# Optimization experiments

Hardware: AMD Instinct MI355X
Metric: run time of the kernel (lower is better)

Reference implementation:

```python
import jax, jax.numpy as jnp
import numpy as np

B, S, D, H, DFF = 2, 2048, 768, 12, 3072
DK = D // H
EPS = 1e-6


def setup_inputs() -> dict:
    key = jax.random.key(0)
    ks = jax.random.split(key, 12)
    n = lambda k, shp: jax.random.normal(k, shp, jnp.float32) * 0.02
    return {
        "x": jax.random.normal(ks[0], (B, S, D), jnp.float32),
        "mask": jax.random.randint(ks[1], (1, 1, S, S), 0, 2).astype(jnp.int32),
        "wq": n(ks[2], (D, D)), "bq": jnp.zeros((D,), jnp.float32),
        "wk": n(ks[3], (D, D)), "bk": jnp.zeros((D,), jnp.float32),
        "wv": n(ks[4], (D, D)), "bv": jnp.zeros((D,), jnp.float32),
        "wo": n(ks[5], (D, D)), "bo": jnp.zeros((D,), jnp.float32),
        "w1": n(ks[6], (D, DFF)), "b1": jnp.zeros((DFF,), jnp.float32),
        "w2": n(ks[7], (DFF, D)), "b2": jnp.zeros((D,), jnp.float32),
        "alpha1": jnp.ones((D,), jnp.float32), "beta1": jnp.zeros((D,), jnp.float32),
        "alpha2": jnp.ones((D,), jnp.float32), "beta2": jnp.zeros((D,), jnp.float32),
    }


def _layernorm(x, alpha, bias):
    # Faithful to source: unbiased std (ddof=1) and eps added to std, not var.
    mean = x.mean(axis=-1, keepdims=True)
    var = jnp.sum((x - mean) ** 2, axis=-1, keepdims=True) / (x.shape[-1] - 1)
    return alpha * (x - mean) / (jnp.sqrt(var) + EPS) + bias


def reference(x, mask, wq, bq, wk, bk, wv, bv, wo, bo, w1, b1, w2, b2,
              alpha1, beta1, alpha2, beta2):
    # --- residual 1: pre-norm self-attention ---
    h = _layernorm(x, alpha1, beta1)
    q = (h @ wq + bq).reshape(B, S, H, DK).transpose(0, 2, 1, 3)  # [B,H,S,DK]
    k = (h @ wk + bk).reshape(B, S, H, DK).transpose(0, 2, 1, 3)
    v = (h @ wv + bv).reshape(B, S, H, DK).transpose(0, 2, 1, 3)
    scores = jnp.einsum('bhsd,bhtd->bhst', q, k) / jnp.sqrt(jnp.float32(DK))
    scores = jnp.where(mask == 0, jnp.float32(-1e9), scores)
    attn = jax.nn.softmax(scores, axis=-1)
    o = jnp.einsum('bhst,bhtd->bhsd', attn, v)
    o = o.transpose(0, 2, 1, 3).reshape(B, S, D)
    x = x + (o @ wo + bo)
    # --- residual 2: pre-norm FFN ---
    h2 = _layernorm(x, alpha2, beta2)
    ff = jnp.maximum(h2 @ w1 + b1, 0.0) @ w2 + b2
    return x + ff
```

## Files before the change

### kernel.cpp

```cpp
#include <hip/hip_runtime.h>

typedef unsigned short u16;
typedef unsigned int u32;
typedef unsigned long long u64;
typedef __attribute__((ext_vector_type(8))) short bf16x8;
typedef __attribute__((ext_vector_type(4))) float f32x4;
typedef __attribute__((ext_vector_type(2))) unsigned int u32x2;

#define SEQ 2048
#define DM  768
#define NH  12
#define NB  2
#define LDQ (3 * DM)

#define SCALE_Q 0.180336879f
#define NEGB   -1.44269504e9f

__device__ __forceinline__ float bf2f(u16 u) {
  union { u32 i; float f; } v; v.i = ((u32)u) << 16; return v.f;
}
__device__ __forceinline__ u16 f2bf(float f) {
  union { float f; u32 i; } v; v.f = f;
  u32 r = v.i + 0x7FFFu + ((v.i >> 16) & 1u);
  return (u16)(r >> 16);
}
__device__ __forceinline__ void gl_lds16(const u16* g, u16* l) {
  __builtin_amdgcn_global_load_lds(
      (const __attribute__((address_space(1))) unsigned int*)g,
      (__attribute__((address_space(3))) unsigned int*)l, 16, 0, 0);
}
template<int N> __device__ __forceinline__ void wait_vmcnt() {
  if constexpr (N == 0) asm volatile("s_waitcnt vmcnt(0)" ::: "memory");
  else if constexpr (N == 3) asm volatile("s_waitcnt vmcnt(3)" ::: "memory");
  else if constexpr (N == 4) asm volatile("s_waitcnt vmcnt(4)" ::: "memory");
}

__global__ __launch_bounds__(256) void prep_kernel(
    const float* __restrict__ wq, const float* __restrict__ wk,
    const float* __restrict__ wv, const float* __restrict__ wo,
    const float* __restrict__ w1, const float* __restrict__ w2,
    const float* __restrict__ bq, const float* __restrict__ bk,
    const float* __restrict__ bv, const int* __restrict__ mask,
    u16* __restrict__ wqkvt, u16* __restrict__ wot,
    u16* __restrict__ w1t, u16* __restrict__ w2t,
    float* __restrict__ bqkv, u64* __restrict__ mbitsT) {
  __shared__ float t[32][33];
  const int j = blockIdx.x, tid = threadIdx.x;
  const float* in = nullptr; u16* out = nullptr;
  int R = 0, C = 0, bx = 0, by = 0; float sc = 1.0f;
  if (j < 2304) {
    int which = j / 576, local = j % 576;
    in = which == 0 ? wq : which == 1 ? wk : which == 2 ? wv : wo;
    out = which == 3 ? wot : wqkvt + (size_t)which * DM * DM;
    sc = (which == 0) ? SCALE_Q : 1.0f;
    R = DM; C = DM; bx = local % 24; by = local / 24;
  } else if (j < 4608) {
    int local = j - 2304;
    in = w1; out = w1t; R = DM; C = 3072; bx = local % 96; by = local / 96;
  } else if (j < 6912) {
    int local = j - 4608;
    in = w2; out = w2t; R = 3072; C = DM; bx = local % 24; by = local / 24;
  } else if (j < 6921) {
    int i = (j - 6912) * 256 + tid;
    float v = (i < DM) ? bq[i] * SCALE_Q : (i < 2 * DM ? bk[i - DM] : bv[i - 2 * DM]);
    bqkv[i] = v;
    return;
  } else {
    int wid = (j - 6921) * 4 + (tid >> 6);
    int lane = tid & 63;
    int row = wid >> 5, word = wid & 31;
    int m = mask[(long)row * SEQ + word * 64 + lane];
    u64 bb = __ballot(m != 0);
    if (lane == 0) mbitsT[(long)word * SEQ + row] = bb;
    return;
  }
  long r0 = (long)by * 32, c0 = (long)bx * 32;
  int lc = tid & 31, wr = tid >> 5;
#pragma unroll
  for (int i = 0; i < 4; i++) {
    int row = wr + i * 8;
    t[row][lc] = in[(r0 + row) * C + c0 + lc];
  }
  __syncthreads();
#pragma unroll
  for (int i = 0; i < 4; i++) {
    int row = wr + i * 8;
    out[(c0 + row) * R + r0 + lc] = f2bf(t[lc][row] * sc);
  }
}

__global__ __launch_bounds__(256) void transpose_kernel(
    const u16* __restrict__ in, u16* __restrict__ out, int ldin, int R, int C) {
  __shared__ u16 t[32][33];
  long r0 = (long)blockIdx.y * 32, c0 = (long)blockIdx.x * 32;
  int lc = threadIdx.x & 31, wr = threadIdx.x >> 5;
#pragma unroll
  for (int i = 0; i < 4; i++) {
    int row = wr + i * 8;
    t[row][lc] = in[(r0 + row) * (long)ldin + c0 + lc];
  }
  __syncthreads();
#pragma unroll
  for (int i = 0; i < 4; i++) {
    int row = wr + i * 8;
    out[(c0 + row) * R + r0 + lc] = t[lc][row];
  }
}

__global__ __launch_bounds__(256) void ln_kernel(
    const float* __restrict__ x, const float* __restrict__ alpha,
    const float* __restrict__ beta, u16* __restrict__ out) {
  long row = blockIdx.x;
  const float* xr = x + row * DM;
  int tid = threadIdx.x;
  float v[3];
  float s = 0.f, sq = 0.f;
#pragma unroll
  for (int i = 0; i < 3; i++) {
    v[i] = xr[tid + i * 256];
    s += v[i]; sq += v[i] * v[i];
  }
#pragma unroll
  for (int off = 32; off >= 1; off >>= 1) {
    s += __shfl_down(s, off, 64);
    sq += __shfl_down(sq, off, 64);
  }
  __shared__ float ss[4], ssq[4];
  int wave = tid >> 6;
  if ((tid & 63) == 0) { ss[wave] = s; ssq[wave] = sq; }
  __syncthreads();
  float ts = ss[0] + ss[1] + ss[2] + ss[3];
  float tsq = ssq[0] + ssq[1] + ssq[2] + ssq[3];
  float mean = ts * (1.0f / (float)DM);
  float var = fmaxf((tsq - ts * mean) * (1.0f / (float)(DM - 1)), 0.0f);
  float inv = 1.0f / (sqrtf(var) + 1e-6f);
#pragma unroll
  for (int i = 0; i < 3; i++) {
    int c = tid + i * 256;
    out[row * DM + c] = f2bf(alpha[c] * (v[i] - mean) * inv + beta[c]);
  }
}

template<int BN>
__global__ __launch_bounds__(256, 2) void gemm_bt_kernel(
    const u16* __restrict__ A, const u16* __restrict__ Bt,
    const float* __restrict__ bias, const float* res,
    u16* Cb, float* Cf, int M, int N, int K, int relu, int nx) {
  constexpr int NJ = BN / 32;
  constexpr int L = (BN == 128) ? 4 : 3;
  __shared__ __align__(16) u16 As[3][128][32];
  __shared__ __align__(16) u16 Bs[3][BN][32];
  const int tid = threadIdx.x;
  const int lane = tid & 63, wave = tid >> 6;
  const int g = lane >> 4, lr = lane & 15;
  const int wm = (wave >> 1) * 64, wn = (wave & 1) * (BN / 2);
  const int o = blockIdx.x;
  const int wg = (o & 7) * ((int)gridDim.x >> 3) + (o >> 3);
  const int bx = wg % nx, by = wg / nx;
  const long m0 = (long)by * 128;
  const long n0 = (long)bx * BN;
  const int srow = tid >> 2;
  const int scol = (tid & 3) * 8;

  const u16* aSrc = A + (m0 + srow) * K + scol;
  const u16* bSrc = Bt + (n0 + srow) * K + scol;

  auto STAGE = [&](int buf, int t) {
    const int k0 = t * 32;
    gl_lds16(aSrc + k0, &As[buf][srow][scol]);
    gl_lds16(aSrc + (long)64 * K + k0, &As[buf][srow + 64][scol]);
    gl_lds16(bSrc + k0, &Bs[buf][srow][scol]);
    if (BN == 128) gl_lds16(bSrc + (long)64 * K + k0, &Bs[buf][srow + 64][scol]);
  };

  f32x4 acc[4][NJ];
#pragma unroll
  for (int i = 0; i < 4; i++)
#pragma unroll
    for (int j = 0; j < NJ; j++) acc[i][j] = (f32x4)0.0f;

  const int nk = K / 32;
  STAGE(0, 0);
  STAGE(1, 1);
  for (int t = 0; t < nk; t++) {
    const int cur = t % 3;
    if (t + 1 < nk) wait_vmcnt<L>(); else wait_vmcnt<0>();
    __builtin_amdgcn_sched_barrier(0);
    __builtin_amdgcn_s_barrier();
    bf16x8 af[4], bfr[NJ];
#pragma unroll
    for (int i = 0; i < 4; i++) af[i] = *(const bf16x8*)&As[cur][wm + i * 16 + lr][g * 8];
#pragma unroll
    for (int j = 0; j < NJ; j++) bfr[j] = *(const bf16x8*)&Bs[cur][wn + j * 16 + lr][g * 8];
#pragma unroll
    for (int i = 0; i < 4; i++)
#pragma unroll
      for (int j = 0; j < NJ; j++)
        acc[i][j] = __builtin_amdgcn_mfma_f32_16x16x32_bf16(af[i], bfr[j], acc[i][j], 0, 0, 0);
    if (t + 2 < nk) STAGE((t + 2) % 3, t + 2);
  }
#pragma unroll
  for (int j = 0; j < NJ; j++) {
    long col = n0 + wn + j * 16 + lr;
    float bv = bias[col];
#pragma unroll
    for (int i = 0; i < 4; i++) {
#pragma unroll
      for (int r = 0; r < 4; r++) {
        long row = m0 + wm + i * 16 + g * 4 + r;
        float v = acc[i][j][r] + bv;
        if (res) v += res[row * N + col];
        if (relu) v = fmaxf(v, 0.0f);
        if (Cb) Cb[row * N + col] = f2bf(v);
        else    Cf[row * N + col] = v;
      }
    }
  }
}

__global__ __launch_bounds__(256, 3) void attn_kernel(
    const u16* __restrict__ qkv, const u16* __restrict__ vt,
    const u64* __restrict__ mbitsT, u16* __restrict__ o_) {
  __shared__ __align__(16) u16 Ks[2][64][64];
  __shared__ __align__(16) u16 Vs[2][64][64];
  __shared__ __align__(16) u32 Ps32[4][16][32];
  const int o = blockIdx.x;
  const int wg = (o & 7) * 96 + (o >> 3);
  const int qt = wg & 31, h = (wg >> 5) % NH, b = wg / (32 * NH);
  const int tid = threadIdx.x;
  const int lane = tid & 63, wave = tid >> 6;
  const int g = lane >> 4, lr = lane & 15;
  const int qr0 = qt * 64 + wave * 16;

  const u16* q = qkv;
  const u16* k = qkv + DM;

  const long qbase = ((long)(b * SEQ + qr0 + lr)) * LDQ + h * 64;
  bf16x8 qf0 = *(const bf16x8*)(q + qbase + g * 8);
  bf16x8 qf1 = *(const bf16x8*)(q + qbase + 32 + g * 8);

  bf16x8 onesf;
#pragma unroll
  for (int j = 0; j < 8; j++) onesf[j] = (short)0x3F80;

  f32x4 lsum = (f32x4)0.0f;
  f32x4 oacc[4];
#pragma unroll
  for (int d = 0; d < 4; d++) oacc[d] = (f32x4)0.0f;

  const int strow = tid >> 3;
  const int stcolb = (tid & 7) * 16;
  const int swzb = stcolb ^ ((strow & 7) << 4);
  const u16* ksrc = k + (long)b * SEQ * LDQ + h * 64 + (swzb >> 1);
  const u16* vsrc = vt + ((long)(h * 64 + strow)) * (NB * SEQ) + (long)b * SEQ + (swzb >> 1);
  const int sc16 = stcolb >> 1;

  auto STAGE = [&](int buf, int kt) {
    const u16* kr = ksrc + (long)(kt * 64 + strow) * LDQ;
    gl_lds16(kr, &Ks[buf][strow][sc16]);
    gl_lds16(kr + (long)32 * LDQ, &Ks[buf][strow + 32][sc16]);
    const u16* vr = vsrc + kt * 64;
    gl_lds16(vr, &Vs[buf][strow][sc16]);
    gl_lds16(vr + 32 * (NB * SEQ), &Vs[buf][strow + 32][sc16]);
  };

  const int rs = (lr & 7) << 3;
  const int c0 = (g * 8) ^ rs;
  const int c1 = (32 + g * 8) ^ rs;

  const u64* mrow = mbitsT + (qr0 + lr);
  const int pswz = (lr & 7) << 2;
  const int pb0 = (4 * g) ^ pswz;
  const int pb1 = (16 + 4 * g) ^ pswz;

  STAGE(0, 0);
  __syncthreads();
  for (int kt = 0; kt < SEQ / 64; kt++) {
    const int cur = kt & 1;
    if (kt + 1 < SEQ / 64) STAGE(cur ^ 1, kt + 1);
    u64 mb = mrow[(long)kt * SEQ];

    f32x4 sf[4];
    __builtin_amdgcn_s_setprio(1);
#pragma unroll
    for (int n = 0; n < 4; n++) {
      bf16x8 kb0 = *(const bf16x8*)&Ks[cur][n * 16 + lr][c0];
      bf16x8 kb1 = *(const bf16x8*)&Ks[cur][n * 16 + lr][c1];
      sf[n] = __builtin_amdgcn_mfma_f32_16x16x32_bf16(kb0, qf0, (f32x4)0.0f, 0, 0, 0);
      sf[n] = __builtin_amdgcn_mfma_f32_16x16x32_bf16(kb1, qf1, sf[n], 0, 0, 0);
    }
    __builtin_amdgcn_s_setprio(0);
    u64 tsh = mb >> (4 * g);
    u32 mlo = (u32)tsh, mhi = (u32)(tsh >> 32);
#pragma unroll
    for (int n = 0; n < 4; n++) {
      u32 w = (n < 2) ? mlo : mhi;
#pragma unroll
      for (int r = 0; r < 4; r++) {
        u32 bit = 1u << (16 * (n & 1) + r);
        sf[n][r] = (w & bit) ? sf[n][r] : NEGB;
      }
    }
#pragma unroll
    for (int n = 0; n < 4; n++) {
      union { float f; u32 i; } p0, p1, p2, p3;
      p0.f = exp2f(sf[n][0]); p1.f = exp2f(sf[n][1]);
      p2.f = exp2f(sf[n][2]); p3.f = exp2f(sf[n][3]);
      u32 w0 = (p1.i & 0xFFFF0000u) | (p0.i >> 16);
      u32 w1 = (p3.i & 0xFFFF0000u) | (p2.i >> 16);
      int widx = (8 * n + 2 * g) ^ pswz;
      *(u32x2*)&Ps32[wave][lr][widx] = (u32x2){w0, w1};
    }
    asm volatile("" ::: "memory");
    bf16x8 pf0 = *(const bf16x8*)&Ps32[wave][lr][pb0];
    bf16x8 pf1 = *(const bf16x8*)&Ps32[wave][lr][pb1];
    __builtin_amdgcn_s_setprio(1);
    lsum = __builtin_amdgcn_mfma_f32_16x16x32_bf16(onesf, pf0, lsum, 0, 0, 0);
    lsum = __builtin_amdgcn_mfma_f32_16x16x32_bf16(onesf, pf1, lsum, 0, 0, 0);
#pragma unroll
    for (int db = 0; db < 4; db++) {
      bf16x8 v0 = *(const bf16x8*)&Vs[cur][db * 16 + lr][c0];
      bf16x8 v1 = *(const bf16x8*)&Vs[cur][db * 16 + lr][c1];
      oacc[db] = __builtin_amdgcn_mfma_f32_16x16x32_bf16(v0, pf0, oacc[db], 0, 0, 0);
      oacc[db] = __builtin_amdgcn_mfma_f32_16x16x32_bf16(v1, pf1, oacc[db], 0, 0, 0);
    }
    __builtin_amdgcn_s_setprio(0);
    __syncthreads();
  }
  float inv = 1.0f / lsum[0];
  long row = (long)b * SEQ + qr0 + lr;
#pragma unroll
  for (int db = 0; db < 4; db++) {
    u32 lo = ((u32)f2bf(oacc[db][1] * inv) << 16) | f2bf(oacc[db][0] * inv);
    u32 hi = ((u32)f2bf(oacc[db][3] * inv) << 16) | f2bf(oacc[db][2] * inv);
    *(u32x2*)(o_ + row * DM + h * 64 + db * 16 + g * 4) = (u32x2){lo, hi};
  }
}

extern "C" void kernel_launch(void* const* d_in, const int* in_sizes, int n_in,
                              void* d_out, int out_size, void* d_ws, size_t ws_size,
                              hipStream_t stream) {
  const float* x      = (const float*)d_in[0];
  const int*   mask   = (const int*)d_in[1];
  const float* wq     = (const float*)d_in[2];
  const float* bq     = (const float*)d_in[3];
  const float* wk     = (const float*)d_in[4];
  const float* bk     = (const float*)d_in[5];
  const float* wv     = (const float*)d_in[6];
  const float* bv     = (const float*)d_in[7];
  const float* wo     = (const float*)d_in[8];
  const float* bo     = (const float*)d_in[9];
  const float* w1     = (const float*)d_in[10];
  const float* b1     = (const float*)d_in[11];
  const float* w2     = (const float*)d_in[12];
  const float* b2     = (const float*)d_in[13];
  const float* alpha1 = (const float*)d_in[14];
  const float* beta1  = (const float*)d_in[15];
  const float* alpha2 = (const float*)d_in[16];
  const float* beta2  = (const float*)d_in[17];
  float* outf = (float*)d_out;

  char* ws = (char*)d_ws;
  size_t off = 0;
  auto alloc = [&](size_t bytes) {
    void* p = ws + off;
    off += (bytes + 255) & ~(size_t)255;
    return p;
  };
  const size_t DD = (size_t)DM * DM * 2;
  const size_t DF = (size_t)DM * 3072 * 2;
  const size_t ROWS = (size_t)NB * SEQ;
  const size_t ACT = ROWS * DM * 2;

  u16* wqkvt = (u16*)alloc(3 * DD);
  u16* wot   = (u16*)alloc(DD);
  u16* w1t   = (u16*)alloc(DF);
  u16* w2t   = (u16*)alloc(DF);
  float* bqkv = (float*)alloc(3 * DM * 4);
  u64* mbitsT = (u64*)alloc((size_t)(SEQ / 64) * SEQ * 8);
  u16* h     = (u16*)alloc(ACT);
  u16* qkv   = (u16*)alloc(ROWS * 3 * DM * 2);
  u16* vtb   = (u16*)alloc(ACT);
  u16* ob    = (u16*)alloc(ACT);
  u16* fb = qkv;
  u16* h2 = h;
  float* x1 = outf;

  dim3 blk(256);
  prep_kernel<<<dim3(23305), blk, 0, stream>>>(wq, wk, wv, wo, w1, w2, bq, bk, bv,
                                               mask, wqkvt, wot, w1t, w2t, bqkv, mbitsT);

  ln_kernel<<<ROWS, blk, 0, stream>>>(x, alpha1, beta1, h);
  gemm_bt_kernel<128><<<dim3(576), blk, 0, stream>>>(h, wqkvt, bqkv, nullptr, qkv, nullptr, 4096, 3 * DM, 768, 0, 18);
  transpose_kernel<<<dim3(24, 128), blk, 0, stream>>>(qkv + 2 * DM, vtb, LDQ, 4096, 768);
  attn_kernel<<<dim3(32 * NH * NB), blk, 0, stream>>>(qkv, vtb, mbitsT, ob);
  gemm_bt_kernel<64><<<dim3(384), blk, 0, stream>>>(ob, wot, bo, x, nullptr, x1, 4096, 768, 768, 0, 12);
  ln_kernel<<<ROWS, blk, 0, stream>>>(x1, alpha2, beta2, h2);
  gemm_bt_kernel<128><<<dim3(768), blk, 0, stream>>>(h2, w1t, b1, nullptr, fb, nullptr, 4096, 3072, 768, 1, 24);
  gemm_bt_kernel<64><<<dim3(384), blk, 0, stream>>>(fb, w2t, b2, x1, nullptr, outf, 4096, 768, 3072, 0, 12);
}
```

Baseline: 220.7 us.

## Pipeline attention K/V staging with explicit vmcnt waits and prefetch mask

Restructures the attention loop so the next tile's K/V async loads and mask word are issued first. Then a partial vmcnt wait retires only the current tile's loads before a raw s_barrier, replacing __syncthreads, which waits for all outstanding loads. The P scratch buffer is padded to 36 words instead of using an XOR swizzle, and the bf16 packing uses a byte-permute instruction. The aim is to overlap global-to-LDS loads with compute and cut ALU work. It depends on the vmcnt count matching the number of loads issued.

```diff
diff --git a/kernel.cpp b/kernel.cpp
--- a/kernel.cpp
+++ b/kernel.cpp
@@ -33,6 +33,7 @@
   if constexpr (N == 0) asm volatile("s_waitcnt vmcnt(0)" ::: "memory");
   else if constexpr (N == 3) asm volatile("s_waitcnt vmcnt(3)" ::: "memory");
   else if constexpr (N == 4) asm volatile("s_waitcnt vmcnt(4)" ::: "memory");
+  else if constexpr (N == 5) asm volatile("s_waitcnt vmcnt(5)" ::: "memory");
 }
 
 __global__ __launch_bounds__(256) void prep_kernel(
@@ -223,7 +224,7 @@
     const u64* __restrict__ mbitsT, u16* __restrict__ o_) {
   __shared__ __align__(16) u16 Ks[2][64][64];
   __shared__ __align__(16) u16 Vs[2][64][64];
-  __shared__ __align__(16) u32 Ps32[4][16][32];
+  __shared__ __align__(16) u32 Ps32[4][16][36];
   const int o = blockIdx.x;
   const int wg = (o & 7) * 96 + (o >> 3);
   const int qt = wg & 31, h = (wg >> 5) % NH, b = wg / (32 * NH);
@@ -231,6 +232,7 @@
   const int lane = tid & 63, wave = tid >> 6;
   const int g = lane >> 4, lr = lane & 15;
   const int qr0 = qt * 64 + wave * 16;
+  const int NT = SEQ / 64;
 
   const u16* q = qkv;
   const u16* k = qkv + DM;
@@ -269,16 +271,21 @@
   const int c1 = (32 + g * 8) ^ rs;
 
   const u64* mrow = mbitsT + (qr0 + lr);
-  const int pswz = (lr & 7) << 2;
-  const int pb0 = (4 * g) ^ pswz;
-  const int pb1 = (16 + 4 * g) ^ pswz;
-
+
+  u64 mb_cur = mrow[0];
   STAGE(0, 0);
-  __syncthreads();
-  for (int kt = 0; kt < SEQ / 64; kt++) {
+  for (int kt = 0; kt < NT; kt++) {
     const int cur = kt & 1;
-    if (kt + 1 < SEQ / 64) STAGE(cur ^ 1, kt + 1);
-    u64 mb = mrow[(long)kt * SEQ];
+    u64 mb_new = 0;
+    if (kt + 1 < NT) {
+      mb_new = mrow[(long)(kt + 1) * SEQ];
+      STAGE(cur ^ 1, kt + 1);
+      wait_vmcnt<5>();
+    } else {
+      wait_vmcnt<0>();
+    }
+    __builtin_amdgcn_sched_barrier(0);
+    __builtin_amdgcn_s_barrier();
 
     f32x4 sf[4];
     __builtin_amdgcn_s_setprio(1);
@@ -290,7 +297,7 @@
       sf[n] = __builtin_amdgcn_mfma_f32_16x16x32_bf16(kb1, qf1, sf[n], 0, 0, 0);
     }
     __builtin_amdgcn_s_setprio(0);
-    u64 tsh = mb >> (4 * g);
+    u64 tsh = mb_cur >> (4 * g);
     u32 mlo = (u32)tsh, mhi = (u32)(tsh >> 32);
 #pragma unroll
     for (int n = 0; n < 4; n++) {
@@ -306,14 +313,13 @@
       union { float f; u32 i; } p0, p1, p2, p3;
       p0.f = exp2f(sf[n][0]); p1.f = exp2f(sf[n][1]);
       p2.f = exp2f(sf[n][2]); p3.f = exp2f(sf[n][3]);
-      u32 w0 = (p1.i & 0xFFFF0000u) | (p0.i >> 16);
-      u32 w1 = (p3.i & 0xFFFF0000u) | (p2.i >> 16);
-      int widx = (8 * n + 2 * g) ^ pswz;
-      *(u32x2*)&Ps32[wave][lr][widx] = (u32x2){w0, w1};
+      u32 w0 = __builtin_amdgcn_perm(p1.i, p0.i, 0x07060302u);
+      u32 w1 = __builtin_amdgcn_perm(p3.i, p2.i, 0x07060302u);
+      *(u32x2*)&Ps32[wave][lr][8 * n + 2 * g] = (u32x2){w0, w1};
     }
     asm volatile("" ::: "memory");
-    bf16x8 pf0 = *(const bf16x8*)&Ps32[wave][lr][pb0];
-    bf16x8 pf1 = *(const bf16x8*)&Ps32[wave][lr][pb1];
+    bf16x8 pf0 = *(const bf16x8*)&Ps32[wave][lr][4 * g];
+    bf16x8 pf1 = *(const bf16x8*)&Ps32[wave][lr][16 + 4 * g];
     __builtin_amdgcn_s_setprio(1);
     lsum = __builtin_amdgcn_mfma_f32_16x16x32_bf16(onesf, pf0, lsum, 0, 0, 0);
     lsum = __builtin_amdgcn_mfma_f32_16x16x32_bf16(onesf, pf1, lsum, 0, 0, 0);
@@ -325,7 +331,9 @@
       oacc[db] = __builtin_amdgcn_mfma_f32_16x16x32_bf16(v1, pf1, oacc[db], 0, 0, 0);
     }
     __builtin_amdgcn_s_setprio(0);
-    __syncthreads();
+    __builtin_amdgcn_sched_barrier(0);
+    __builtin_amdgcn_s_barrier();
+    mb_cur = mb_new;
   }
   float inv = 1.0f / lsum[0];
   long row = (long)b * SEQ + qr0 + lr;
```

New measurement: 219.7 us. No clear change (-0.5%).
